# Optimization experiments

Hardware: AMD Instinct MI355X
Metric: run time of the kernel (lower is better)

The kernel has to match this reference:

```python
import jax, jax.numpy as jnp
import numpy as np

B, N, E = 8, 2048, 1024


def setup_inputs() -> dict:
    key = jax.random.key(0)
    x = jax.random.normal(key, (B, N, E), dtype=jnp.float32)
    pos = jnp.ones((N - 1,), dtype=jnp.float32)
    zero = jnp.ones((1,), dtype=jnp.float32)
    neg = jnp.ones((N - 1,), dtype=jnp.float32)
    return {"x": x, "pos": pos, "zero": zero, "neg": neg}


def reference(x, pos, zero, neg):
    # x: [b, n, e]; Toeplitz matvec via circular FFT convolution of length 2n.
    b, n, e = x.shape
    # circulant kernel: [zero, pos[:n-1], zero, neg[-(n-1):]] -> length 2n
    a = jnp.concatenate([zero, pos[: n - 1], zero, neg[-(n - 1):]])
    # torch: fft(x, 2n, dim=1, norm='ortho')
    y = jnp.fft.fft(x, n=2 * n, axis=1, norm="ortho")  # [b, 2n, e] complex
    # torch: fft(a) with default ('backward') norm, i.e. unnormalized forward
    v = jnp.fft.fft(a)[None, :, None]                   # [1, 2n, 1]
    u = v * y
    out = jnp.fft.ifft(u, n=2 * n, axis=1, norm="ortho")[:, :n, :].real
    return out.astype(x.dtype)
```

## Files before the change

### kernel.cpp

```cpp
#include <hip/hip_runtime.h>
#include <stdint.h>


#define B_ 8
#define N_ 2048
#define NF 4096
#define E_ 1024

__device__ __forceinline__ int P(int n) {
    return n ^ ((n >> 4) & 15) ^ ((n >> 8) & 15) ^ (((n >> 9) & 1) << 4);
}
#define PERM(r) ((((r) & 3) << 2) | ((r) >> 2))

__device__ __forceinline__ unsigned short f32_to_bf16_rne(float f) {
    union { float f; unsigned int u; } cv; cv.f = f;
    unsigned int u = cv.u;
    u += 0x7fffu + ((u >> 16) & 1u);
    return (unsigned short)(u >> 16);
}
__device__ __forceinline__ float bf16_to_f32(unsigned short u) {
    union { unsigned int u; float f; } cv; cv.u = ((unsigned int)u) << 16; return cv.f;
}
__device__ __forceinline__ void cmul(float& ar, float& ai, float br, float bi) {
    float t = ar * br - ai * bi; ai = ar * bi + ai * br; ar = t;
}
__device__ __forceinline__ void cmulc(float& ar, float& ai, float br, float bi) {
    float t = ar * br + ai * bi; ai = ai * br - ar * bi; ar = t;
}

__device__ __forceinline__ void dft4(float& x0r, float& x0i, float& x1r, float& x1i,
                                     float& x2r, float& x2i, float& x3r, float& x3i,
                                     float sg) {
    float t0r = x0r + x2r, t0i = x0i + x2i;
    float t1r = x0r - x2r, t1i = x0i - x2i;
    float t2r = x1r + x3r, t2i = x1i + x3i;
    float t3r = x1r - x3r, t3i = x1i - x3i;
    x0r = t0r + t2r; x0i = t0i + t2i;
    x2r = t0r - t2r; x2i = t0i - t2i;
    x1r = t1r - sg * t3i; x1i = t1i + sg * t3r;
    x3r = t1r + sg * t3i; x3i = t1i - sg * t3r;
}

template<int SG>
__device__ __forceinline__ void dft16_layer1(float* xr, float* xi) {
    const float sg = (float)SG;
#pragma unroll
    for (int n0 = 0; n0 < 4; ++n0)
        dft4(xr[n0], xi[n0], xr[n0 + 4], xi[n0 + 4],
             xr[n0 + 8], xi[n0 + 8], xr[n0 + 12], xi[n0 + 12], sg);
}
template<int SG>
__device__ __forceinline__ void dft16_layer1_pad(float* xr, float* xi) {
    const float sg = (float)SG;
#pragma unroll
    for (int n0 = 0; n0 < 4; ++n0) {
        float ar = xr[n0], ai = xi[n0], br = xr[n0 + 4], bi = xi[n0 + 4];
        xr[n0]      = ar + br;       xi[n0]      = ai + bi;
        xr[n0 + 4]  = ar - sg * bi;  xi[n0 + 4]  = ai + sg * br;
        xr[n0 + 8]  = ar - br;       xi[n0 + 8]  = ai - bi;
        xr[n0 + 12] = ar + sg * bi;  xi[n0 + 12] = ai - sg * br;
    }
}
template<int SG>
__device__ __forceinline__ void dft16_twiddle(float* xr, float* xi) {
    const float sg = (float)SG;
    const float C1 = 0.923879532511286756f;
    const float S1 = 0.382683432365089772f;
    const float H  = 0.707106781186547524f;
    cmul(xr[5],  xi[5],  C1,  sg * S1);
    cmul(xr[9],  xi[9],  H,   sg * H);
    cmul(xr[13], xi[13], S1,  sg * C1);
    cmul(xr[6],  xi[6],  H,   sg * H);
    cmul(xr[10], xi[10], 0.f, sg);
    cmul(xr[14], xi[14], -H,  sg * H);
    cmul(xr[7],  xi[7],  S1,  sg * C1);
    cmul(xr[11], xi[11], -H,  sg * H);
    cmul(xr[15], xi[15], -C1, -sg * S1);
}
template<int SG>
__device__ __forceinline__ void dft16_layer2(float* xr, float* xi) {
    const float sg = (float)SG;
#pragma unroll
    for (int k1 = 0; k1 < 4; ++k1)
        dft4(xr[4 * k1], xi[4 * k1], xr[4 * k1 + 1], xi[4 * k1 + 1],
             xr[4 * k1 + 2], xi[4 * k1 + 2], xr[4 * k1 + 3], xi[4 * k1 + 3], sg);
}
template<int SG>
__device__ __forceinline__ void dft16(float* xr, float* xi) {
    dft16_layer1<SG>(xr, xi);
    dft16_twiddle<SG>(xr, xi);
    dft16_layer2<SG>(xr, xi);
}

template<int L>
__device__ __forceinline__ void fwd_stage_sincos(float2* buf, int t) {
    constexpr int Lq = L / 16;
    int g = t / Lq;
    int j = t - g * Lq;
    int base = g * L + j;
    const float TPI = -6.28318530717958647692f;
    float xr[16], xi[16];
#pragma unroll
    for (int r = 0; r < 16; ++r) {
        float2 v = buf[P(base + r * Lq)];
        xr[r] = v.x; xi[r] = v.y;
    }
    dft16<-1>(xr, xi);
    { float2 v; v.x = xr[0]; v.y = xi[0]; buf[P(base)] = v; }
#pragma unroll
    for (int r = 1; r < 16; ++r) {
        float s, c;
        __sincosf(TPI * (float)(j * r) * (1.f / (float)L), &s, &c);
        float yr = xr[PERM(r)], yi = xi[PERM(r)];
        cmul(yr, yi, c, s);
        float2 v; v.x = yr; v.y = yi;
        buf[P(base + r * Lq)] = v;
    }
}

__global__ __launch_bounds__(256) void prep(const float* __restrict__ x,
                                            const float* __restrict__ pos,
                                            const float* __restrict__ zero,
                                            const float* __restrict__ neg,
                                            unsigned short* __restrict__ xT,
                                            float2* __restrict__ tw4096,
                                            float2* __restrict__ tw256,
                                            float2* __restrict__ V2) {
    __shared__ __align__(16) char smraw[32768];
    const float TPI = -6.28318530717958647692f;
    int blk = blockIdx.x, t = threadIdx.x;
    if (blk < 16) {
        float s, c;
        __sincosf(TPI * (float)(blk * t) * (1.f / 4096.f), &s, &c);
        float2 v; v.x = c; v.y = s;
        tw4096[blk * 256 + t] = v;
    } else if (blk == 16) {
        int r = t >> 4, j = t & 15;
        float s, c;
        __sincosf(TPI * (float)(r * j) * (1.f / 256.f), &s, &c);
        float2 v; v.x = c; v.y = s;
        tw256[t] = v;
    } else if (blk == 17) {
        float2* buf = (float2*)smraw;
#pragma unroll
        for (int it = 0; it < 16; ++it) {
            int n = t + 256 * it;
            float v;
            if (n == 0) v = zero[0];
            else if (n < N_) v = pos[n - 1];
            else if (n == N_) v = zero[0];
            else v = neg[n - (N_ + 1)];
            float2 cc; cc.x = v; cc.y = 0.f;
            buf[P(n)] = cc;
        }
        __syncthreads();
        fwd_stage_sincos<4096>(buf, t); __syncthreads();
        fwd_stage_sincos<256>(buf, t);  __syncthreads();
        fwd_stage_sincos<16>(buf, t);   __syncthreads();
        const float s = 1.f / (float)NF;
#pragma unroll
        for (int it = 0; it < 16; ++it) {
            int n = t + 256 * it;
            float2 c = buf[P(n)];
            c.x *= s; c.y *= s;
            V2[n] = c;
        }
    } else {
        float (*tile)[66] = (float (*)[66])smraw;
        int tid = blk - 18;
        int e0 = (tid & 15) * 64;
        int j0 = ((tid >> 4) & 31) * 64;
        int b  = tid >> 9;
        int e4 = t & 15, jr = t >> 4;
#pragma unroll
        for (int it = 0; it < 4; ++it) {
            int j = jr + it * 16;
            const float4 v = *(const float4*)(x + ((size_t)(b * N_ + j0 + j) * E_) + e0 + e4 * 4);
            tile[e4 * 4 + 0][j] = v.x;
            tile[e4 * 4 + 1][j] = v.y;
            tile[e4 * 4 + 2][j] = v.z;
            tile[e4 * 4 + 3][j] = v.w;
        }
        __syncthreads();
        int j2 = (t & 31) * 2, er = t >> 5;
#pragma unroll
        for (int it = 0; it < 8; ++it) {
            int e = er + it * 8;
            float2 v = *(const float2*)&tile[e][j2];
            union { unsigned short s[2]; unsigned int u; } pk;
            pk.s[0] = f32_to_bf16_rne(v.x);
            pk.s[1] = f32_to_bf16_rne(v.y);
            *(unsigned int*)(xT + ((size_t)(b * E_ + e0 + e)) * N_ + j0 + j2) = pk.u;
        }
    }
}

__global__ __launch_bounds__(256) void fft_conv(const unsigned short* __restrict__ xT,
                                                const float2* __restrict__ tw4096,
                                                const float2* __restrict__ tw256,
                                                const float2* __restrict__ V2,
                                                float* __restrict__ out) {
    __shared__ float2 buf[NF];
    int t = threadIdx.x;
    int bid = blockIdx.x;
    int xcd = bid & 7;
    int q = bid >> 3;
    int b = q >> 6;
    int e0 = (xcd * 64 + (q & 63)) * 2;

    const unsigned short* r0 = xT + ((size_t)(b * E_ + e0)) * N_;
    const unsigned short* r1 = r0 + N_;

    float xr[16], xi[16];

#pragma unroll
    for (int r = 0; r < 8; ++r) {
        int n = t + 256 * r;
        xr[r] = bf16_to_f32(r0[n]);
        xi[r] = bf16_to_f32(r1[n]);
    }
#pragma unroll
    for (int r = 8; r < 16; ++r) { xr[r] = 0.f; xi[r] = 0.f; }
    dft16_layer1_pad<-1>(xr, xi);
    dft16_twiddle<-1>(xr, xi);
    dft16_layer2<-1>(xr, xi);
    { float2 v; v.x = xr[0]; v.y = xi[0]; buf[P(t)] = v; }
#pragma unroll
    for (int r = 1; r < 16; ++r) {
        float2 w = tw4096[r * 256 + t];
        float yr = xr[PERM(r)], yi = xi[PERM(r)];
        cmul(yr, yi, w.x, w.y);
        float2 v; v.x = yr; v.y = yi;
        buf[P(t + 256 * r)] = v;
    }
    __syncthreads();

    int g = t >> 4, j = t & 15;
    int base = g * 256 + j;
#pragma unroll
    for (int r = 0; r < 16; ++r) {
        float2 v = buf[P(base + 16 * r)];
        xr[r] = v.x; xi[r] = v.y;
    }
    dft16<-1>(xr, xi);
    { float2 v; v.x = xr[0]; v.y = xi[0]; buf[P(base)] = v; }
#pragma unroll
    for (int r = 1; r < 16; ++r) {
        float2 w = tw256[r * 16 + j];
        float yr = xr[PERM(r)], yi = xi[PERM(r)];
        cmul(yr, yi, w.x, w.y);
        float2 v; v.x = yr; v.y = yi;
        buf[P(base + 16 * r)] = v;
    }
    __syncthreads();

    {
        int mb = 16 * t;
#pragma unroll
        for (int r = 0; r < 16; ++r) {
            float2 v = buf[P(mb + r)];
            xr[r] = v.x; xi[r] = v.y;
        }
        dft16<-1>(xr, xi);
#pragma unroll
        for (int r = 0; r < 16; ++r) {
            int p = PERM(r);
            if (p < r) continue;
            if (p == r) {
                float2 vv = V2[mb + r];
                float ar = xr[r], ai = xi[r];
                xr[r] = ar * vv.x - ai * vv.y;
                xi[r] = ar * vv.y + ai * vv.x;
            } else {
                float2 va = V2[mb + r], vb = V2[mb + p];
                float ar = xr[r], ai = xi[r], br = xr[p], bi = xi[p];
                xr[r] = br * va.x - bi * va.y;
                xi[r] = br * va.y + bi * va.x;
                xr[p] = ar * vb.x - ai * vb.y;
                xi[p] = ar * vb.y + ai * vb.x;
            }
        }
        dft16<1>(xr, xi);
#pragma unroll
        for (int r = 0; r < 16; ++r) {
            float2 v; v.x = xr[PERM(r)]; v.y = xi[PERM(r)];
            buf[P(mb + r)] = v;
        }
    }
    __syncthreads();

#pragma unroll
    for (int r = 0; r < 16; ++r) {
        float2 v = buf[P(base + 16 * r)];
        xr[r] = v.x; xi[r] = v.y;
    }
#pragma unroll
    for (int r = 1; r < 16; ++r) {
        float2 w = tw256[r * 16 + j];
        cmulc(xr[r], xi[r], w.x, w.y);
    }
    dft16<1>(xr, xi);
#pragma unroll
    for (int r = 0; r < 16; ++r) {
        float2 v; v.x = xr[PERM(r)]; v.y = xi[PERM(r)];
        buf[P(base + 16 * r)] = v;
    }
    __syncthreads();

#pragma unroll
    for (int r = 0; r < 16; ++r) {
        float2 v = buf[P(t + 256 * r)];
        xr[r] = v.x; xi[r] = v.y;
    }
#pragma unroll
    for (int r = 1; r < 16; ++r) {
        float2 w = tw4096[r * 256 + t];
        cmulc(xr[r], xi[r], w.x, w.y);
    }
    dft16_layer1<1>(xr, xi);
    dft16_twiddle<1>(xr, xi);
    float* ob = out + ((size_t)b * N_) * E_ + e0;
#pragma unroll
    for (int k1 = 0; k1 < 4; ++k1) {
        float a0r = xr[4 * k1],     a0i = xi[4 * k1];
        float a1r = xr[4 * k1 + 1], a1i = xi[4 * k1 + 1];
        float a2r = xr[4 * k1 + 2], a2i = xi[4 * k1 + 2];
        float a3r = xr[4 * k1 + 3], a3i = xi[4 * k1 + 3];
        float t0r = a0r + a2r, t0i = a0i + a2i;
        float t1r = a0r - a2r, t1i = a0i - a2i;
        float t2r = a1r + a3r, t2i = a1i + a3i;
        float t3r = a1r - a3r, t3i = a1i - a3i;
        float2 v0; v0.x = t0r + t2r; v0.y = t0i + t2i;
        float2 v1; v1.x = t1r - t3i; v1.y = t1i + t3r;
        *(float2*)(ob + (size_t)(t + 256 * k1) * E_)       = v0;
        *(float2*)(ob + (size_t)(t + 256 * (k1 + 4)) * E_) = v1;
    }
}

__global__ __launch_bounds__(256) void naive_toep(const float* __restrict__ x,
                                                  const float* __restrict__ pos,
                                                  const float* __restrict__ zero,
                                                  const float* __restrict__ neg,
                                                  float* __restrict__ out) {
    int bid = blockIdx.x;
    int e   = (bid & 3) * 256 + threadIdx.x;
    int k   = (bid >> 2) & (N_ - 1);
    int b   = bid >> 13;
    float zv = zero[0];
    float acc = 0.f;
    const float* xb = x + (size_t)b * N_ * E_ + e;
    for (int jj = 0; jj < N_; ++jj) {
        float c = (jj < k) ? pos[k - jj - 1] : (jj == k) ? zv : neg[N_ - 1 - jj + k];
        acc += c * xb[(size_t)jj * E_];
    }
    out[((size_t)(b * N_ + k)) * E_ + e] = acc;
}

extern "C" void kernel_launch(void* const* d_in, const int* in_sizes, int n_in,
                              void* d_out, int out_size, void* d_ws, size_t ws_size,
                              hipStream_t stream) {
    const float* x    = (const float*)d_in[0];
    const float* pos  = (const float*)d_in[1];
    const float* zero = (const float*)d_in[2];
    const float* neg  = (const float*)d_in[3];
    float* out = (float*)d_out;

    const size_t needX = (size_t)B_ * E_ * N_ * sizeof(unsigned short);
    const size_t need  = needX + (2 * (size_t)NF + 256) * sizeof(float2);
    if (ws_size >= need) {
        unsigned short* xT = (unsigned short*)d_ws;
        float2* tw4096 = (float2*)((char*)d_ws + needX);
        float2* tw256  = tw4096 + NF;
        float2* V2     = tw256 + 256;
        prep<<<18 + 4096, 256, 0, stream>>>(x, pos, zero, neg, xT, tw4096, tw256, V2);
        fft_conv<<<4096, 256, 0, stream>>>(xT, tw4096, tw256, V2, out);
    } else {
        naive_toep<<<65536, 256, 0, stream>>>(x, pos, zero, neg, out);
    }
}
```

Measured before the change: 197.8 us.

## Process four channels per FFT block with interleaved bf16 pairs and float4 stores

The prep kernel now writes the bf16 transpose with adjacent channel pairs interleaved into 32-bit words. Each fft_conv block then handles two complex sequences (four real channels) using two shared buffers, so the grid is halved. Twiddle loads, V2 loads and address math are shared across both sequences, and output stores widen to float4. The cost is double the shared memory per block (64KB) and twice the register arrays, which may reduce occupancy or cause spills.

New measurement: 177.0 us. -10.5%, faster.

```diff
diff --git a/kernel.cpp b/kernel.cpp
--- a/kernel.cpp
+++ b/kernel.cpp
@@ -122,7 +122,7 @@
                                             const float* __restrict__ pos,
                                             const float* __restrict__ zero,
                                             const float* __restrict__ neg,
-                                            unsigned short* __restrict__ xT,
+                                            uint32_t* __restrict__ xP,
                                             float2* __restrict__ tw4096,
                                             float2* __restrict__ tw256,
                                             float2* __restrict__ V2) {
@@ -182,56 +182,62 @@
             tile[e4 * 4 + 3][j] = v.w;
         }
         __syncthreads();
-        int j2 = (t & 31) * 2, er = t >> 5;
+        int jj = t & 63, ur = t >> 6;
 #pragma unroll
         for (int it = 0; it < 8; ++it) {
-            int e = er + it * 8;
-            float2 v = *(const float2*)&tile[e][j2];
-            union { unsigned short s[2]; unsigned int u; } pk;
-            pk.s[0] = f32_to_bf16_rne(v.x);
-            pk.s[1] = f32_to_bf16_rne(v.y);
-            *(unsigned int*)(xT + ((size_t)(b * E_ + e0 + e)) * N_ + j0 + j2) = pk.u;
-        }
-    }
-}
-
-__global__ __launch_bounds__(256) void fft_conv(const unsigned short* __restrict__ xT,
+            int u = ur + it * 4;
+            union { unsigned short s[2]; uint32_t w; } pk;
+            pk.s[0] = f32_to_bf16_rne(tile[2 * u][jj]);
+            pk.s[1] = f32_to_bf16_rne(tile[2 * u + 1][jj]);
+            xP[((size_t)(b * 512 + (e0 >> 1) + u)) * N_ + j0 + jj] = pk.w;
+        }
+    }
+}
+
+__global__ __launch_bounds__(256) void fft_conv(const uint32_t* __restrict__ xP,
                                                 const float2* __restrict__ tw4096,
                                                 const float2* __restrict__ tw256,
                                                 const float2* __restrict__ V2,
                                                 float* __restrict__ out) {
-    __shared__ float2 buf[NF];
+    __shared__ float2 buf0[NF];
+    __shared__ float2 buf1[NF];
     int t = threadIdx.x;
     int bid = blockIdx.x;
     int xcd = bid & 7;
     int q = bid >> 3;
-    int b = q >> 6;
-    int e0 = (xcd * 64 + (q & 63)) * 2;
-
-    const unsigned short* r0 = xT + ((size_t)(b * E_ + e0)) * N_;
-    const unsigned short* r1 = r0 + N_;
-
-    float xr[16], xi[16];
+    int b = q >> 5;
+    int quad = xcd * 32 + (q & 31);
+    const uint32_t* g0 = xP + ((size_t)(b * 512 + quad * 2)) * N_;
+    const uint32_t* g1 = g0 + N_;
+
+    float x0r[16], x0i[16], x1r[16], x1i[16];
 
 #pragma unroll
     for (int r = 0; r < 8; ++r) {
         int n = t + 256 * r;
-        xr[r] = bf16_to_f32(r0[n]);
-        xi[r] = bf16_to_f32(r1[n]);
-    }
-#pragma unroll
-    for (int r = 8; r < 16; ++r) { xr[r] = 0.f; xi[r] = 0.f; }
-    dft16_layer1_pad<-1>(xr, xi);
-    dft16_twiddle<-1>(xr, xi);
-    dft16_layer2<-1>(xr, xi);
-    { float2 v; v.x = xr[0]; v.y = xi[0]; buf[P(t)] = v; }
+        uint32_t u0 = g0[n], u1 = g1[n];
+        x0r[r] = bf16_to_f32((unsigned short)(u0 & 0xffff));
+        x0i[r] = bf16_to_f32((unsigned short)(u0 >> 16));
+        x1r[r] = bf16_to_f32((unsigned short)(u1 & 0xffff));
+        x1i[r] = bf16_to_f32((unsigned short)(u1 >> 16));
+    }
+#pragma unroll
+    for (int r = 8; r < 16; ++r) { x0r[r] = 0.f; x0i[r] = 0.f; x1r[r] = 0.f; x1i[r] = 0.f; }
+    dft16_layer1_pad<-1>(x0r, x0i); dft16_layer1_pad<-1>(x1r, x1i);
+    dft16_twiddle<-1>(x0r, x0i);    dft16_twiddle<-1>(x1r, x1i);
+    dft16_layer2<-1>(x0r, x0i);     dft16_layer2<-1>(x1r, x1i);
+    { float2 v; v.x = x0r[0]; v.y = x0i[0]; buf0[P(t)] = v;
+      float2 w; w.x = x1r[0]; w.y = x1i[0]; buf1[P(t)] = w; }
 #pragma unroll
     for (int r = 1; r < 16; ++r) {
         float2 w = tw4096[r * 256 + t];
-        float yr = xr[PERM(r)], yi = xi[PERM(r)];
-        cmul(yr, yi, w.x, w.y);
-        float2 v; v.x = yr; v.y = yi;
-        buf[P(t + 256 * r)] = v;
+        int a = P(t + 256 * r);
+        float y0r = x0r[PERM(r)], y0i = x0i[PERM(r)];
+        cmul(y0r, y0i, w.x, w.y);
+        float2 v0; v0.x = y0r; v0.y = y0i; buf0[a] = v0;
+        float y1r = x1r[PERM(r)], y1i = x1i[PERM(r)];
+        cmul(y1r, y1i, w.x, w.y);
+        float2 v1; v1.x = y1r; v1.y = y1i; buf1[a] = v1;
     }
     __syncthreads();
 
@@ -239,18 +245,23 @@
     int base = g * 256 + j;
 #pragma unroll
     for (int r = 0; r < 16; ++r) {
-        float2 v = buf[P(base + 16 * r)];
-        xr[r] = v.x; xi[r] = v.y;
-    }
-    dft16<-1>(xr, xi);
-    { float2 v; v.x = xr[0]; v.y = xi[0]; buf[P(base)] = v; }
+        int a = P(base + 16 * r);
+        float2 v0 = buf0[a]; x0r[r] = v0.x; x0i[r] = v0.y;
+        float2 v1 = buf1[a]; x1r[r] = v1.x; x1i[r] = v1.y;
+    }
+    dft16<-1>(x0r, x0i); dft16<-1>(x1r, x1i);
+    { float2 v; v.x = x0r[0]; v.y = x0i[0]; buf0[P(base)] = v;
+      float2 w; w.x = x1r[0]; w.y = x1i[0]; buf1[P(base)] = w; }
 #pragma unroll
     for (int r = 1; r < 16; ++r) {
         float2 w = tw256[r * 16 + j];
-        float yr = xr[PERM(r)], yi = xi[PERM(r)];
-        cmul(yr, yi, w.x, w.y);
-        float2 v; v.x = yr; v.y = yi;
-        buf[P(base + 16 * r)] = v;
+        int a = P(base + 16 * r);
+        float y0r = x0r[PERM(r)], y0i = x0i[PERM(r)];
+        cmul(y0r, y0i, w.x, w.y);
+        float2 v0; v0.x = y0r; v0.y = y0i; buf0[a] = v0;
+        float y1r = x1r[PERM(r)], y1i = x1i[PERM(r)];
+        cmul(y1r, y1i, w.x, w.y);
+        float2 v1; v1.x = y1r; v1.y = y1i; buf1[a] = v1;
     }
     __syncthreads();
 
@@ -258,82 +269,103 @@
         int mb = 16 * t;
 #pragma unroll
         for (int r = 0; r < 16; ++r) {
-            float2 v = buf[P(mb + r)];
-            xr[r] = v.x; xi[r] = v.y;
-        }
-        dft16<-1>(xr, xi);
+            int a = P(mb + r);
+            float2 v0 = buf0[a]; x0r[r] = v0.x; x0i[r] = v0.y;
+            float2 v1 = buf1[a]; x1r[r] = v1.x; x1i[r] = v1.y;
+        }
+        dft16<-1>(x0r, x0i); dft16<-1>(x1r, x1i);
 #pragma unroll
         for (int r = 0; r < 16; ++r) {
             int p = PERM(r);
             if (p < r) continue;
             if (p == r) {
                 float2 vv = V2[mb + r];
-                float ar = xr[r], ai = xi[r];
-                xr[r] = ar * vv.x - ai * vv.y;
-                xi[r] = ar * vv.y + ai * vv.x;
+                float ar = x0r[r], ai = x0i[r];
+                x0r[r] = ar * vv.x - ai * vv.y; x0i[r] = ar * vv.y + ai * vv.x;
+                ar = x1r[r]; ai = x1i[r];
+                x1r[r] = ar * vv.x - ai * vv.y; x1i[r] = ar * vv.y + ai * vv.x;
             } else {
                 float2 va = V2[mb + r], vb = V2[mb + p];
-                float ar = xr[r], ai = xi[r], br = xr[p], bi = xi[p];
-                xr[r] = br * va.x - bi * va.y;
-                xi[r] = br * va.y + bi * va.x;
-                xr[p] = ar * vb.x - ai * vb.y;
-                xi[p] = ar * vb.y + ai * vb.x;
+                float ar = x0r[r], ai = x0i[r], br = x0r[p], bi = x0i[p];
+                x0r[r] = br * va.x - bi * va.y; x0i[r] = br * va.y + bi * va.x;
+                x0r[p] = ar * vb.x - ai * vb.y; x0i[p] = ar * vb.y + ai * vb.x;
+                ar = x1r[r]; ai = x1i[r]; br = x1r[p]; bi = x1i[p];
+                x1r[r] = br * va.x - bi * va.y; x1i[r] = br * va.y + bi * va.x;
+                x1r[p] = ar * vb.x - ai * vb.y; x1i[p] = ar * vb.y + ai * vb.x;
             }
         }
-        dft16<1>(xr, xi);
+        dft16<1>(x0r, x0i); dft16<1>(x1r, x1i);
 #pragma unroll
         for (int r = 0; r < 16; ++r) {
-            float2 v; v.x = xr[PERM(r)]; v.y = xi[PERM(r)];
-            buf[P(mb + r)] = v;
+            int a = P(mb + r);
+            float2 v0; v0.x = x0r[PERM(r)]; v0.y = x0i[PERM(r)]; buf0[a] = v0;
+            float2 v1; v1.x = x1r[PERM(r)]; v1.y = x1i[PERM(r)]; buf1[a] = v1;
         }
     }
     __syncthreads();
 
 #pragma unroll
     for (int r = 0; r < 16; ++r) {
-        float2 v = buf[P(base + 16 * r)];
-        xr[r] = v.x; xi[r] = v.y;
+        int a = P(base + 16 * r);
+        float2 v0 = buf0[a]; x0r[r] = v0.x; x0i[r] = v0.y;
+        float2 v1 = buf1[a]; x1r[r] = v1.x; x1i[r] = v1.y;
     }
 #pragma unroll
     for (int r = 1; r < 16; ++r) {
         float2 w = tw256[r * 16 + j];
-        cmulc(xr[r], xi[r], w.x, w.y);
-    }
-    dft16<1>(xr, xi);
+        cmulc(x0r[r], x0i[r], w.x, w.y);
+        cmulc(x1r[r], x1i[r], w.x, w.y);
+    }
+    dft16<1>(x0r, x0i); dft16<1>(x1r, x1i);
 #pragma unroll
     for (int r = 0; r < 16; ++r) {
-        float2 v; v.x = xr[PERM(r)]; v.y = xi[PERM(r)];
-        buf[P(base + 16 * r)] = v;
+        int a = P(base + 16 * r);
+        float2 v0; v0.x = x0r[PERM(r)]; v0.y = x0i[PERM(r)]; buf0[a] = v0;
+        float2 v1; v1.x = x1r[PERM(r)]; v1.y = x1i[PERM(r)]; buf1[a] = v1;
     }
     __syncthreads();
 
 #pragma unroll
     for (int r = 0; r < 16; ++r) {
-        float2 v = buf[P(t + 256 * r)];
-        xr[r] = v.x; xi[r] = v.y;
+        int a = P(t + 256 * r);
+        float2 v0 = buf0[a]; x0r[r] = v0.x; x0i[r] = v0.y;
+        float2 v1 = buf1[a]; x1r[r] = v1.x; x1i[r] = v1.y;
     }
 #pragma unroll
     for (int r = 1; r < 16; ++r) {
         float2 w = tw4096[r * 256 + t];
-        cmulc(xr[r], xi[r], w.x, w.y);
-    }
-    dft16_layer1<1>(xr, xi);
-    dft16_twiddle<1>(xr, xi);
-    float* ob = out + ((size_t)b * N_) * E_ + e0;
+        cmulc(x0r[r], x0i[r], w.x, w.y);
+        cmulc(x1r[r], x1i[r], w.x, w.y);
+    }
+    dft16_layer1<1>(x0r, x0i); dft16_layer1<1>(x1r, x1i);
+    dft16_twiddle<1>(x0r, x0i); dft16_twiddle<1>(x1r, x1i);
+    float* ob = out + ((size_t)b * N_) * E_ + quad * 4;
 #pragma unroll
     for (int k1 = 0; k1 < 4; ++k1) {
-        float a0r = xr[4 * k1],     a0i = xi[4 * k1];
-        float a1r = xr[4 * k1 + 1], a1i = xi[4 * k1 + 1];
-        float a2r = xr[4 * k1 + 2], a2i = xi[4 * k1 + 2];
-        float a3r = xr[4 * k1 + 3], a3i = xi[4 * k1 + 3];
+        float a0r = x0r[4 * k1],     a0i = x0i[4 * k1];
+        float a1r = x0r[4 * k1 + 1], a1i = x0i[4 * k1 + 1];
+        float a2r = x0r[4 * k1 + 2], a2i = x0i[4 * k1 + 2];
+        float a3r = x0r[4 * k1 + 3], a3i = x0i[4 * k1 + 3];
         float t0r = a0r + a2r, t0i = a0i + a2i;
         float t1r = a0r - a2r, t1i = a0i - a2i;
         float t2r = a1r + a3r, t2i = a1i + a3i;
         float t3r = a1r - a3r, t3i = a1i - a3i;
-        float2 v0; v0.x = t0r + t2r; v0.y = t0i + t2i;
-        float2 v1; v1.x = t1r - t3i; v1.y = t1i + t3r;
-        *(float2*)(ob + (size_t)(t + 256 * k1) * E_)       = v0;
-        *(float2*)(ob + (size_t)(t + 256 * (k1 + 4)) * E_) = v1;
+        float s0v0r = t0r + t2r, s0v0i = t0i + t2i;
+        float s0v1r = t1r - t3i, s0v1i = t1i + t3r;
+        a0r = x1r[4 * k1];     a0i = x1i[4 * k1];
+        a1r = x1r[4 * k1 + 1]; a1i = x1i[4 * k1 + 1];
+        a2r = x1r[4 * k1 + 2]; a2i = x1i[4 * k1 + 2];
+        a3r = x1r[4 * k1 + 3]; a3i = x1i[4 * k1 + 3];
+        t0r = a0r + a2r; t0i = a0i + a2i;
+        t1r = a0r - a2r; t1i = a0i - a2i;
+        t2r = a1r + a3r; t2i = a1i + a3i;
+        t3r = a1r - a3r; t3i = a1i - a3i;
+        float s1v0r = t0r + t2r, s1v0i = t0i + t2i;
+        float s1v1r = t1r - t3i, s1v1i = t1i + t3r;
+        float4 w0; w0.x = s0v0r; w0.y = s0v0i; w0.z = s1v0r; w0.w = s1v0i;
+        float4 w1; w1.x = s0v1r; w1.y = s0v1i; w1.z = s1v1r; w1.w = s1v1i;
+        *(float4*)(ob + (size_t)(t + 256 * k1) * E_)       = w0;
+        *(float4*)(ob + (size_t)(t + 256 * (k1 + 4)) * E_) = w1;
     }
 }
 
@@ -365,15 +397,15 @@
     const float* neg  = (const float*)d_in[3];
     float* out = (float*)d_out;
 
-    const size_t needX = (size_t)B_ * E_ * N_ * sizeof(unsigned short);
+    const size_t needX = (size_t)B_ * 512 * N_ * sizeof(uint32_t);
     const size_t need  = needX + (2 * (size_t)NF + 256) * sizeof(float2);
     if (ws_size >= need) {
-        unsigned short* xT = (unsigned short*)d_ws;
+        uint32_t* xP   = (uint32_t*)d_ws;
         float2* tw4096 = (float2*)((char*)d_ws + needX);
         float2* tw256  = tw4096 + NF;
         float2* V2     = tw256 + 256;
-        prep<<<18 + 4096, 256, 0, stream>>>(x, pos, zero, neg, xT, tw4096, tw256, V2);
-        fft_conv<<<4096, 256, 0, stream>>>(xT, tw4096, tw256, V2, out);
+        prep<<<18 + 4096, 256, 0, stream>>>(x, pos, zero, neg, xP, tw4096, tw256, V2);
+        fft_conv<<<2048, 256, 0, stream>>>(xP, tw4096, tw256, V2, out);
     } else {
         naive_toep<<<65536, 256, 0, stream>>>(x, pos, zero, neg, out);
     }
```
